# Optimization experiments

Hardware: AMD Instinct MI355X
Metric: run time of the kernel (lower is better)

## Reference

```python
import jax, jax.numpy as jnp
import numpy as np

SEQ = 16384
D = 1024


def setup_inputs() -> dict:
    key = jax.random.key(0)
    k1, k2, k3, k4 = jax.random.split(key, 4)
    return {
        "G_M1": jax.random.normal(k1, (SEQ, D), dtype=jnp.float32),
        "G_M2": jax.random.normal(k2, (SEQ, D), dtype=jnp.float32),
        "wp1": jax.random.normal(k3, (1, D), dtype=jnp.float32),
        "wp2": jax.random.normal(k4, (1, D), dtype=jnp.float32),
    }


def reference(G_M1, G_M2, wp1, wp2):
    # Original: per-row tensordot(wp1, G_M1[i][:, None]) -> [1,1], concat along
    # axis 1 -> p1 of shape [1, SEQ]; same for p2; softmax over the seq axis.
    # This is exactly a single matvec per head followed by softmax.
    p1 = jnp.einsum("od,sd->os", wp1, G_M1)  # [1, SEQ]
    p2 = jnp.einsum("od,sd->os", wp2, G_M2)  # [1, SEQ]
    p1_pred = jax.nn.softmax(p1, axis=-1)
    p2_pred = jax.nn.softmax(p2, axis=-1)
    return (p1_pred, p2_pred)
```

## Files before the change

kernel.cpp:

```cpp
#include <hip/hip_runtime.h>
#include <hip/hip_bf16.h>
#include <math.h>

#define SEQ 16384
#define D   1024

__global__ __launch_bounds__(256) void dot_kernel(
    const float* __restrict__ g1, const float* __restrict__ g2,
    const float* __restrict__ wp1, const float* __restrict__ wp2,
    float* __restrict__ logits) {
  const int lane   = threadIdx.x & 63;
  const int wave   = (blockIdx.x * blockDim.x + threadIdx.x) >> 6;
  const int nwaves = (gridDim.x * blockDim.x) >> 6;

  float4 w1v[4], w2v[4];
  const float4* wp1v = (const float4*)wp1;
  const float4* wp2v = (const float4*)wp2;
#pragma unroll
  for (int j = 0; j < 4; ++j) {
    w1v[j] = wp1v[lane + 64 * j];
    w2v[j] = wp2v[lane + 64 * j];
  }

  for (int r = wave; r < 2 * SEQ; r += nwaves) {
    const bool head0 = (r < SEQ);
    const float* rowp = head0 ? (g1 + (size_t)r * D)
                              : (g2 + (size_t)(r - SEQ) * D);
    const float4* rowv = (const float4*)rowp;
    float acc = 0.0f;
#pragma unroll
    for (int j = 0; j < 4; ++j) {
      float4 a = rowv[lane + 64 * j];
      float4 w = head0 ? w1v[j] : w2v[j];
      acc = fmaf(a.x, w.x, acc);
      acc = fmaf(a.y, w.y, acc);
      acc = fmaf(a.z, w.z, acc);
      acc = fmaf(a.w, w.w, acc);
    }
#pragma unroll
    for (int off = 32; off > 0; off >>= 1)
      acc += __shfl_xor(acc, off, 64);
    if (lane == 0) logits[r] = acc;
  }
}

__global__ __launch_bounds__(1024) void softmax_kernel(
    const float* __restrict__ logits, float* __restrict__ out) {
  const int head = blockIdx.x;
  const float* x = logits + head * SEQ;
  float* y = out + head * SEQ;
  const int tid  = threadIdx.x;
  const int lane = tid & 63;
  const int wid  = tid >> 6;

  float vals[16];
  float m = -INFINITY;
#pragma unroll
  for (int i = 0; i < 16; ++i) {
    float v = x[tid + i * 1024];
    vals[i] = v;
    m = fmaxf(m, v);
  }

  __shared__ float sm[16];
  __shared__ float ss[16];

#pragma unroll
  for (int off = 32; off > 0; off >>= 1)
    m = fmaxf(m, __shfl_xor(m, off, 64));
  if (lane == 0) sm[wid] = m;
  __syncthreads();
  float bm = sm[0];
#pragma unroll
  for (int i = 1; i < 16; ++i) bm = fmaxf(bm, sm[i]);

  float s = 0.0f;
#pragma unroll
  for (int i = 0; i < 16; ++i) {
    vals[i] = __expf(vals[i] - bm);
    s += vals[i];
  }
#pragma unroll
  for (int off = 32; off > 0; off >>= 1)
    s += __shfl_xor(s, off, 64);
  if (lane == 0) ss[wid] = s;
  __syncthreads();
  float bs = 0.0f;
#pragma unroll
  for (int i = 0; i < 16; ++i) bs += ss[i];
  const float inv = 1.0f / bs;

#pragma unroll
  for (int i = 0; i < 16; ++i)
    y[tid + i * 1024] = vals[i] * inv;
}

extern "C" void kernel_launch(void* const* d_in, const int* in_sizes, int n_in,
                              void* d_out, int out_size, void* d_ws, size_t ws_size,
                              hipStream_t stream) {
  const float* g1  = (const float*)d_in[0];
  const float* g2  = (const float*)d_in[1];
  const float* wp1 = (const float*)d_in[2];
  const float* wp2 = (const float*)d_in[3];
  float* out    = (float*)d_out;
  float* logits = (float*)d_ws;

  dot_kernel<<<2048, 256, 0, stream>>>(g1, g2, wp1, wp2, logits);
  softmax_kernel<<<2, 1024, 0, stream>>>(logits, out);
}
```

Before: 149.6 us.

## Fuse per-block softmax partials into dot kernel and split softmax into stats and normalize

The dot kernel now has each wave compute four consecutive rows at once, so more loads are in flight, instead of looping grid-stride over one row at a time. It also computes per-block online-softmax partials (max and rescaled sum) and writes them out. A small stats kernel merges these into a global max and inverse sum per head. A 32-block normalize kernel then applies exp and scale. This replaces the old 2-block softmax that had each thread do 16 serial loads, at the cost of a third kernel launch and some extra exp work.

Result: slower. 153.3 us (+2.5%).

```diff
diff --git a/kernel.cpp b/kernel.cpp
--- a/kernel.cpp
+++ b/kernel.cpp
@@ -4,95 +4,122 @@
 
 #define SEQ 16384
 #define D   1024
+#define NBLK_DOT 2048
+#define WAVES_PER_BLK 4
 
-__global__ __launch_bounds__(256) void dot_kernel(
+__global__ __launch_bounds__(256) void dot_partial_kernel(
     const float* __restrict__ g1, const float* __restrict__ g2,
     const float* __restrict__ wp1, const float* __restrict__ wp2,
-    float* __restrict__ logits) {
-  const int lane   = threadIdx.x & 63;
-  const int wave   = (blockIdx.x * blockDim.x + threadIdx.x) >> 6;
-  const int nwaves = (gridDim.x * blockDim.x) >> 6;
+    float* __restrict__ logits,
+    float* __restrict__ blk_m, float* __restrict__ blk_s) {
+  const int lane = threadIdx.x & 63;
+  const int wid  = threadIdx.x >> 6;
+  const int w    = blockIdx.x * WAVES_PER_BLK + wid;
+  const int r0   = w * 4;
+  const bool head1 = (r0 >= SEQ);
+  const float* g  = head1 ? g2 : g1;
+  const float* wp = head1 ? wp2 : wp1;
+  const int row0  = head1 ? (r0 - SEQ) : r0;
 
-  float4 w1v[4], w2v[4];
-  const float4* wp1v = (const float4*)wp1;
-  const float4* wp2v = (const float4*)wp2;
+  const float4* wpv = (const float4*)wp;
+  float4 wv[4];
 #pragma unroll
-  for (int j = 0; j < 4; ++j) {
-    w1v[j] = wp1v[lane + 64 * j];
-    w2v[j] = wp2v[lane + 64 * j];
+  for (int k = 0; k < 4; ++k) wv[k] = wpv[lane + 64 * k];
+
+  const float4* rv = (const float4*)(g + (size_t)row0 * D);
+  float acc0 = 0.f, acc1 = 0.f, acc2 = 0.f, acc3 = 0.f;
+#pragma unroll
+  for (int k = 0; k < 4; ++k) {
+    const int o = lane + 64 * k;
+    float4 a0 = rv[o];
+    float4 a1 = rv[o + 256];
+    float4 a2 = rv[o + 512];
+    float4 a3 = rv[o + 768];
+    float4 wk = wv[k];
+    acc0 = fmaf(a0.x, wk.x, fmaf(a0.y, wk.y, fmaf(a0.z, wk.z, fmaf(a0.w, wk.w, acc0))));
+    acc1 = fmaf(a1.x, wk.x, fmaf(a1.y, wk.y, fmaf(a1.z, wk.z, fmaf(a1.w, wk.w, acc1))));
+    acc2 = fmaf(a2.x, wk.x, fmaf(a2.y, wk.y, fmaf(a2.z, wk.z, fmaf(a2.w, wk.w, acc2))));
+    acc3 = fmaf(a3.x, wk.x, fmaf(a3.y, wk.y, fmaf(a3.z, wk.z, fmaf(a3.w, wk.w, acc3))));
+  }
+#pragma unroll
+  for (int off = 32; off > 0; off >>= 1) {
+    acc0 += __shfl_xor(acc0, off, 64);
+    acc1 += __shfl_xor(acc1, off, 64);
+    acc2 += __shfl_xor(acc2, off, 64);
+    acc3 += __shfl_xor(acc3, off, 64);
+  }
+  if (lane == 0) {
+    *(float4*)(logits + r0) = make_float4(acc0, acc1, acc2, acc3);
   }
 
-  for (int r = wave; r < 2 * SEQ; r += nwaves) {
-    const bool head0 = (r < SEQ);
-    const float* rowp = head0 ? (g1 + (size_t)r * D)
-                              : (g2 + (size_t)(r - SEQ) * D);
-    const float4* rowv = (const float4*)rowp;
-    float acc = 0.0f;
-#pragma unroll
-    for (int j = 0; j < 4; ++j) {
-      float4 a = rowv[lane + 64 * j];
-      float4 w = head0 ? w1v[j] : w2v[j];
-      acc = fmaf(a.x, w.x, acc);
-      acc = fmaf(a.y, w.y, acc);
-      acc = fmaf(a.z, w.z, acc);
-      acc = fmaf(a.w, w.w, acc);
-    }
-#pragma unroll
-    for (int off = 32; off > 0; off >>= 1)
-      acc += __shfl_xor(acc, off, 64);
-    if (lane == 0) logits[r] = acc;
+  float mw = fmaxf(fmaxf(acc0, acc1), fmaxf(acc2, acc3));
+  float sw = __expf(acc0 - mw) + __expf(acc1 - mw) +
+             __expf(acc2 - mw) + __expf(acc3 - mw);
+
+  __shared__ float lm[WAVES_PER_BLK], ls[WAVES_PER_BLK];
+  if (lane == 0) { lm[wid] = mw; ls[wid] = sw; }
+  __syncthreads();
+  if (threadIdx.x == 0) {
+    float M = fmaxf(fmaxf(lm[0], lm[1]), fmaxf(lm[2], lm[3]));
+    float S = ls[0] * __expf(lm[0] - M) + ls[1] * __expf(lm[1] - M) +
+              ls[2] * __expf(lm[2] - M) + ls[3] * __expf(lm[3] - M);
+    blk_m[blockIdx.x] = M;
+    blk_s[blockIdx.x] = S;
   }
 }
 
-__global__ __launch_bounds__(1024) void softmax_kernel(
-    const float* __restrict__ logits, float* __restrict__ out) {
-  const int head = blockIdx.x;
-  const float* x = logits + head * SEQ;
-  float* y = out + head * SEQ;
+__global__ __launch_bounds__(1024) void stats_kernel(
+    const float* __restrict__ blk_m, const float* __restrict__ blk_s,
+    float* __restrict__ stats) {
+  const int h    = blockIdx.x;
   const int tid  = threadIdx.x;
   const int lane = tid & 63;
   const int wid  = tid >> 6;
 
-  float vals[16];
-  float m = -INFINITY;
-#pragma unroll
-  for (int i = 0; i < 16; ++i) {
-    float v = x[tid + i * 1024];
-    vals[i] = v;
-    m = fmaxf(m, v);
-  }
+  float m = blk_m[h * 1024 + tid];
+  float s = blk_s[h * 1024 + tid];
 
-  __shared__ float sm[16];
-  __shared__ float ss[16];
+  __shared__ float sm[16], ssum[16];
 
+  float mm = m;
 #pragma unroll
   for (int off = 32; off > 0; off >>= 1)
-    m = fmaxf(m, __shfl_xor(m, off, 64));
-  if (lane == 0) sm[wid] = m;
+    mm = fmaxf(mm, __shfl_xor(mm, off, 64));
+  if (lane == 0) sm[wid] = mm;
   __syncthreads();
-  float bm = sm[0];
+  float M = sm[0];
 #pragma unroll
-  for (int i = 1; i < 16; ++i) bm = fmaxf(bm, sm[i]);
+  for (int i = 1; i < 16; ++i) M = fmaxf(M, sm[i]);
 
-  float s = 0.0f;
-#pragma unroll
-  for (int i = 0; i < 16; ++i) {
-    vals[i] = __expf(vals[i] - bm);
-    s += vals[i];
-  }
+  float c = s * __expf(m - M);
 #pragma unroll
   for (int off = 32; off > 0; off >>= 1)
-    s += __shfl_xor(s, off, 64);
-  if (lane == 0) ss[wid] = s;
+    c += __shfl_xor(c, off, 64);
+  if (lane == 0) ssum[wid] = c;
   __syncthreads();
-  float bs = 0.0f;
+  if (tid == 0) {
+    float S = 0.f;
 #pragma unroll
-  for (int i = 0; i < 16; ++i) bs += ss[i];
-  const float inv = 1.0f / bs;
+    for (int i = 0; i < 16; ++i) S += ssum[i];
+    stats[2 * h]     = M;
+    stats[2 * h + 1] = 1.0f / S;
+  }
+}
 
-#pragma unroll
-  for (int i = 0; i < 16; ++i)
-    y[tid + i * 1024] = vals[i] * inv;
+__global__ __launch_bounds__(256) void normalize_kernel(
+    const float4* __restrict__ logits4, const float* __restrict__ stats,
+    float4* __restrict__ out4) {
+  const int i = blockIdx.x * blockDim.x + threadIdx.x;
+  const int h = i >> 12;
+  const float M    = stats[2 * h];
+  const float invS = stats[2 * h + 1];
+  float4 v = logits4[i];
+  float4 o;
+  o.x = __expf(v.x - M) * invS;
+  o.y = __expf(v.y - M) * invS;
+  o.z = __expf(v.z - M) * invS;
+  o.w = __expf(v.w - M) * invS;
+  out4[i] = o;
 }
 
 extern "C" void kernel_launch(void* const* d_in, const int* in_sizes, int n_in,
@@ -102,9 +129,16 @@
   const float* g2  = (const float*)d_in[1];
   const float* wp1 = (const float*)d_in[2];
   const float* wp2 = (const float*)d_in[3];
-  float* out    = (float*)d_out;
+  float* out = (float*)d_out;
+
   float* logits = (float*)d_ws;
+  float* blk_m  = logits + 2 * SEQ;
+  float* blk_s  = blk_m + NBLK_DOT;
+  float* stats  = blk_s + NBLK_DOT;
 
-  dot_kernel<<<2048, 256, 0, stream>>>(g1, g2, wp1, wp2, logits);
-  softmax_kernel<<<2, 1024, 0, stream>>>(logits, out);
+  dot_partial_kernel<<<NBLK_DOT, 256, 0, stream>>>(g1, g2, wp1, wp2,
+                                                   logits, blk_m, blk_s);
+  stats_kernel<<<2, 1024, 0, stream>>>(blk_m, blk_s, stats);
+  normalize_kernel<<<32, 256, 0, stream>>>((const float4*)logits, stats,
+                                           (float4*)out);
 }
```
